# Performance work log

Hardware: AMD Instinct MI355X
Metric: run time of the kernel (lower is better)

Reference implementation:

```python
import jax, jax.numpy as jnp
import numpy as np

_OFF = [(dz, dy, dx) for dz in (-1, 0, 1) for dy in (-1, 0, 1) for dx in (-1, 0, 1)]
_K3 = [(kz, ky, kx) for kz in range(3) for ky in range(3) for kx in range(3)]


def _key(c, dims):
    D, H, W = dims
    return ((c[:, 0].astype(np.int64) * D + c[:, 1]) * H + c[:, 2]) * W + c[:, 3]


def _dedupe(c, dims):
    k = _key(c, dims)
    _, idx = np.unique(k, return_index=True)
    return c[np.sort(idx)]


def _make_lookup(coords, dims):
    D, H, W = dims
    keys = _key(coords, dims)
    order = np.argsort(keys)
    skeys = keys[order]

    def query(qc):
        valid = ((qc[:, 1] >= 0) & (qc[:, 1] < D) & (qc[:, 2] >= 0) & (qc[:, 2] < H)
                 & (qc[:, 3] >= 0) & (qc[:, 3] < W))
        qk = _key(np.where(valid[:, None], qc, 0), dims)
        pos = np.clip(np.searchsorted(skeys, qk), 0, len(skeys) - 1)
        hit = valid & (skeys[pos] == qk)
        return np.where(hit, order[pos], -1).astype(np.int32)
    return query


def _subm_nbr(coords, query):
    nbr = np.empty((len(coords), 27), np.int32)
    for ki, (dz, dy, dx) in enumerate(_OFF):
        qc = coords.copy()
        qc[:, 1] += dz; qc[:, 2] += dy; qc[:, 3] += dx
        nbr[:, ki] = query(qc)
    return nbr


def _down(in_coords, pads, out_dims, in_query):
    # spconv SparseConv3d k=3 s=2: output active set + gather rulebook (in = 2*out - p + k)
    p = np.array(pads)
    cand = []
    for k in _K3:
        t = in_coords[:, 1:] + p - np.array(k)
        m = (t % 2 == 0).all(1)
        o = t[m] // 2
        ok = (o >= 0).all(1) & (o < np.array(out_dims)).all(1)
        cand.append(np.concatenate([in_coords[m][ok][:, :1], o[ok]], 1))
    out_coords = _dedupe(np.concatenate(cand), out_dims)
    nbrd = np.empty((len(out_coords), 27), np.int32)
    for ki, k in enumerate(_K3):
        qc = out_coords.copy()
        qc[:, 1:] = out_coords[:, 1:] * 2 - p + np.array(k)
        nbrd[:, ki] = in_query(qc)
    return out_coords, nbrd


def _inv(in_coords, pads, out_query):
    # inverse conv: for each stride-s input voxel i, gather downsampled voxel o = (i+p-k)/2
    p = np.array(pads)
    nbr = np.full((len(in_coords), 27), -1, np.int32)
    for ki, k in enumerate(_K3):
        t = in_coords[:, 1:] + p - np.array(k)
        div = (t % 2 == 0).all(1)
        qc = in_coords.copy()
        qc[:, 1:] = np.where(div[:, None], t // 2, -1)
        nbr[:, ki] = np.where(div, out_query(qc), -1)
    return nbr


def setup_inputs() -> dict:
    rng = np.random.default_rng(0)
    B, K, P, STD = 4, 160, 128, 3.0
    D1 = (41, 1024, 1024)  # sparse_shape (z, y, x)
    pts = []
    for b in range(B):
        ctr = np.stack([rng.uniform(2, d - 3, K) for d in D1], 1)
        pb = ctr[:, None, :] + rng.normal(0.0, STD, (K, P, 3))
        pb = np.clip(np.rint(pb.reshape(-1, 3)), 0, np.array(D1) - 1).astype(np.int64)
        pts.append(np.concatenate([np.full((len(pb), 1), b, np.int64), pb], 1))
    c1 = _dedupe(np.concatenate(pts), D1)
    D2 = tuple((d + 2 * q - 3) // 2 + 1 for d, q in zip(D1, (1, 1, 1)))
    D3 = tuple((d + 2 * q - 3) // 2 + 1 for d, q in zip(D2, (1, 1, 1)))
    D4 = tuple((d + 2 * q - 3) // 2 + 1 for d, q in zip(D3, (0, 1, 1)))
    q1 = _make_lookup(c1, D1); nbr1 = _subm_nbr(c1, q1)
    c2, nbrd2 = _down(c1, (1, 1, 1), D2, q1); q2 = _make_lookup(c2, D2); nbr2 = _subm_nbr(c2, q2)
    c3, nbrd3 = _down(c2, (1, 1, 1), D3, q2); q3 = _make_lookup(c3, D3); nbr3 = _subm_nbr(c3, q3)
    c4, nbrd4 = _down(c3, (0, 1, 1), D4, q3); q4 = _make_lookup(c4, D4); nbr4 = _subm_nbr(c4, q4)
    nbri4 = _inv(c3, (0, 1, 1), q4)
    nbri3 = _inv(c2, (1, 1, 1), q3)
    nbri2 = _inv(c1, (1, 1, 1), q2)
    N1 = len(c1)
    w = lambda *s: jnp.asarray((0.05 * rng.standard_normal(s)).astype(np.float32))
    bn = lambda n, c: jnp.asarray(np.stack([1.0 + 0.02 * rng.standard_normal((n, c)),
                                            0.02 * rng.standard_normal((n, c))], 1).astype(np.float32))
    return {
        'voxel_feat': jnp.asarray(rng.standard_normal((N1, 4)).astype(np.float32)),
        'Win': w(27, 4, 32),
        'W32': w(10, 27, 32, 32),
        'W64': w(10, 27, 64, 64),
        'Wd3': w(27, 32, 64),
        'W6432': w(3, 27, 64, 32),
        'W12864': w(2, 27, 128, 64),
        'bn32': bn(14, 32),
        'bn64': bn(13, 64),
        'nbr1': jnp.asarray(nbr1), 'nbr2': jnp.asarray(nbr2),
        'nbr3': jnp.asarray(nbr3), 'nbr4': jnp.asarray(nbr4),
        'nbrd2': jnp.asarray(nbrd2), 'nbrd3': jnp.asarray(nbrd3), 'nbrd4': jnp.asarray(nbrd4),
        'nbri4': jnp.asarray(nbri4), 'nbri3': jnp.asarray(nbri3), 'nbri2': jnp.asarray(nbri2),
    }


def _conv(feat, nbr, W):
    # rulebook gather-matmul-scatter: out[n] = sum_k feat[nbr[n,k]] @ W[k]
    out = jnp.zeros((nbr.shape[0], W.shape[-1]), feat.dtype)
    for k in range(27):
        idx = nbr[:, k]
        g = jnp.where((idx >= 0)[:, None], feat[jnp.maximum(idx, 0)], 0.0)
        out = out + g @ W[k]
    return out


def _block(f, nbr, W, sb):  # conv + (folded, eval-mode) BN + ReLU
    return jax.nn.relu(_conv(f, nbr, W) * sb[0] + sb[1])


def _basic(f, nbr, Wa, sa, Wb, sb):  # SparseBasicBlock
    h = jax.nn.relu(_conv(f, nbr, Wa) * sa[0] + sa[1])
    h = _conv(h, nbr, Wb) * sb[0] + sb[1]
    return jax.nn.relu(h + f)


def _reduce(c, oc):  # channel_reduction: view(n, oc, -1).sum(2)
    return c.reshape(c.shape[0], oc, -1).sum(-1)


def _forward(voxel_feat, Win, W32, W64, Wd3, W6432, W12864, bn32, bn64,
             nbr1, nbr2, nbr3, nbr4, nbrd2, nbrd3, nbrd4, nbri4, nbri3, nbri2):
    x = _block(voxel_feat, nbr1, Win, bn32[0])       # conv_input
    x1 = _block(x, nbr1, W32[0], bn32[1])            # conv1
    h = _block(x1, nbrd2, W32[1], bn32[2])           # spconv2 stride-2
    h = _block(h, nbr2, W32[2], bn32[3])
    x2 = _block(h, nbr2, W32[3], bn32[4])
    h = _block(x2, nbrd3, Wd3, bn64[0])              # spconv3 stride-2, 32->64
    h = _block(h, nbr3, W64[0], bn64[1])
    x3 = _block(h, nbr3, W64[1], bn64[2])
    h = _block(x3, nbrd4, W64[2], bn64[3])           # spconv4 stride-2, pad (0,1,1)
    h = _block(h, nbr4, W64[3], bn64[4])
    x4 = _block(h, nbr4, W64[4], bn64[5])
    # UR block 4 (lateral = bottom = x4)
    t = _basic(x4, nbr4, W64[5], bn64[6], W64[6], bn64[7])
    cat = jnp.concatenate([x4, t], 1)                # [N4, 128]
    x = _block(cat, nbr4, W12864[0], bn64[11]) + _reduce(cat, 64)
    xu4 = _block(x, nbri4, W64[7], bn64[8])          # inverseconv -> level 3
    # UR block 3
    t = _basic(x3, nbr3, W64[8], bn64[9], W64[9], bn64[10])
    cat = jnp.concatenate([xu4, t], 1)
    x = _block(cat, nbr3, W12864[1], bn64[12]) + _reduce(cat, 64)
    xu3 = _block(x, nbri3, W6432[0], bn32[11])       # inverseconv -> level 2, 32ch
    # UR block 2
    t = _basic(x2, nbr2, W32[4], bn32[5], W32[5], bn32[6])
    cat = jnp.concatenate([xu3, t], 1)
    x = _block(cat, nbr2, W6432[1], bn32[12]) + _reduce(cat, 32)
    xu2 = _block(x, nbri2, W32[6], bn32[7])          # inverseconv -> level 1
    # UR block 1 (conv_inv = conv5, submanifold at level 1)
    t = _basic(x1, nbr1, W32[7], bn32[8], W32[8], bn32[9])
    cat = jnp.concatenate([xu2, t], 1)
    x = _block(cat, nbr1, W6432[2], bn32[13]) + _reduce(cat, 32)
    return _block(x, nbr1, W32[9], bn32[10])         # conv5 -> unet_voxel_feat [N1, 32]


def reference(voxel_feat, Win, W32, W64, Wd3, W6432, W12864, bn32, bn64,
              nbr1, nbr2, nbr3, nbr4, nbrd2, nbrd3, nbrd4, nbri4, nbri3, nbri2):
    return _forward(voxel_feat, Win, W32, W64, Wd3, W6432, W12864, bn32, bn64,
                    nbr1, nbr2, nbr3, nbr4, nbrd2, nbrd3, nbrd4, nbri4, nbri3, nbri2)
```

## Files before the change

kernel.cpp:

```cpp
#include <hip/hip_runtime.h>


template<int CIN_A, int CIN_B, int COUT, int EPI, bool SPLIT>
__global__ __launch_bounds__(256) void spconv(
    const float* __restrict__ inA,
    const float* __restrict__ inB,
    const int*   __restrict__ nbr,
    const float* __restrict__ W,
    const float* __restrict__ bn,
    const float* __restrict__ skip,
    float*       __restrict__ out,
    float*       __restrict__ pout,
    int N, int KS)
{
    constexpr int CIN   = CIN_A + CIN_B;
    constexpr int BM    = (COUT == 32) ? 128 : 64;
    constexpr int COL_T = COUT / 4;
    constexpr int ROW_T = 256 / COL_T;
    static_assert(ROW_T * 4 == BM, "tile mismatch");
    constexpr int V     = CIN / 4;
    constexpr int GTOT  = BM * V;
    constexpr int GPT   = (GTOT + 255) / 256;
    constexpr int CSTR  = 256 / BM;
    constexpr int WTOT  = CIN * COUT / 4;
    constexpr int WPT   = (WTOT + 255) / 256;

    __shared__ int   s_nbr[BM * 27];
    __shared__ float s_G[CIN][BM];
    __shared__ float s_W[CIN * COUT];

    const int tid = threadIdx.x;
    const int tx  = tid % COL_T;
    const int ty  = tid / COL_T;

    unsigned nwg = gridDim.x;
    unsigned q8 = nwg / 8u, r8 = nwg % 8u;
    unsigned xcd = blockIdx.x % 8u, sub = blockIdx.x / 8u;
    unsigned id = (xcd < r8 ? xcd * (q8 + 1u) : r8 * (q8 + 1u) + (xcd - r8) * q8) + sub;

    int rb, k0, k1, kg;
    if (SPLIT) {
        kg = (int)(id % (unsigned)KS);
        rb = (int)(id / (unsigned)KS);
        int kper = 27 / KS;
        k0 = kg * kper; k1 = k0 + kper;
    } else {
        kg = 0; rb = (int)id; k0 = 0; k1 = 27;
    }
    const int row0 = rb * BM;

    for (int e = tid; e < BM * 27; e += 256) {
        int rr = row0 + e / 27;
        s_nbr[e] = (rr < N) ? nbr[(size_t)row0 * 27 + e] : -1;
    }
    __syncthreads();

    const int gr  = tid % BM;
    const int gc0 = tid / BM;
    float4 gv[GPT];
    float4 wv[WPT];

    auto load_tap = [&](int k) {
        int idx = s_nbr[gr * 27 + k];
        #pragma unroll
        for (int j = 0; j < GPT; ++j) {
            int e = tid + j * 256;
            if ((GTOT % 256 == 0) || e < GTOT) {
                int c4 = gc0 + j * CSTR;
                float4 v = make_float4(0.f, 0.f, 0.f, 0.f);
                if (idx >= 0) {
                    if (CIN_B == 0 || c4 * 4 < CIN_A)
                        v = *(const float4*)(inA + (size_t)idx * CIN_A + c4 * 4);
                    else
                        v = *(const float4*)(inB + (size_t)idx * CIN_B + c4 * 4 - CIN_A);
                }
                gv[j] = v;
            }
        }
        const float4* Wg = (const float4*)(W + (size_t)k * CIN * COUT);
        #pragma unroll
        for (int j = 0; j < WPT; ++j) {
            int e = tid + j * 256;
            if ((WTOT % 256 == 0) || e < WTOT) wv[j] = Wg[e];
        }
    };

    auto store_tap = [&]() {
        #pragma unroll
        for (int j = 0; j < GPT; ++j) {
            int e = tid + j * 256;
            if ((GTOT % 256 == 0) || e < GTOT) {
                int c4 = gc0 + j * CSTR;
                s_G[c4 * 4 + 0][gr] = gv[j].x;
                s_G[c4 * 4 + 1][gr] = gv[j].y;
                s_G[c4 * 4 + 2][gr] = gv[j].z;
                s_G[c4 * 4 + 3][gr] = gv[j].w;
            }
        }
        #pragma unroll
        for (int j = 0; j < WPT; ++j) {
            int e = tid + j * 256;
            if ((WTOT % 256 == 0) || e < WTOT) ((float4*)s_W)[e] = wv[j];
        }
    };

    float acc[4][4] = {};
    load_tap(k0);

    for (int k = k0; k < k1; ++k) {
        __syncthreads();
        store_tap();
        __syncthreads();
        if (k + 1 < k1) load_tap(k + 1);
        #pragma unroll 16
        for (int ci = 0; ci < CIN; ++ci) {
            float4 g = *(const float4*)&s_G[ci][ty * 4];
            float4 w = *(const float4*)&s_W[ci * COUT + tx * 4];
            acc[0][0] += g.x * w.x; acc[0][1] += g.x * w.y; acc[0][2] += g.x * w.z; acc[0][3] += g.x * w.w;
            acc[1][0] += g.y * w.x; acc[1][1] += g.y * w.y; acc[1][2] += g.y * w.z; acc[1][3] += g.y * w.w;
            acc[2][0] += g.z * w.x; acc[2][1] += g.z * w.y; acc[2][2] += g.z * w.z; acc[2][3] += g.z * w.w;
            acc[3][0] += g.w * w.x; acc[3][1] += g.w * w.y; acc[3][2] += g.w * w.z; acc[3][3] += g.w * w.w;
        }
    }

    const int co0 = tx * 4;
    if (SPLIT) {
        #pragma unroll
        for (int i = 0; i < 4; ++i) {
            int rr = row0 + ty * 4 + i;
            if (rr < N) {
                float4 y = make_float4(acc[i][0], acc[i][1], acc[i][2], acc[i][3]);
                *(float4*)(pout + ((size_t)kg * N + rr) * COUT + co0) = y;
            }
        }
    } else {
        float4 sc = *(const float4*)(bn + co0);
        float4 bi = *(const float4*)(bn + COUT + co0);
        #pragma unroll
        for (int i = 0; i < 4; ++i) {
            int rr = row0 + ty * 4 + i;
            if (rr >= N) break;
            float4 y;
            y.x = acc[i][0] * sc.x + bi.x;
            y.y = acc[i][1] * sc.y + bi.y;
            y.z = acc[i][2] * sc.z + bi.z;
            y.w = acc[i][3] * sc.w + bi.w;
            if (EPI == 1) {
                float4 s = *(const float4*)(skip + (size_t)rr * COUT + co0);
                y.x += s.x; y.y += s.y; y.z += s.z; y.w += s.w;
            }
            y.x = fmaxf(y.x, 0.f); y.y = fmaxf(y.y, 0.f);
            y.z = fmaxf(y.z, 0.f); y.w = fmaxf(y.w, 0.f);
            if (EPI == 2) {
                const float* rs = (2 * co0 < CIN_A)
                    ? inA + (size_t)rr * CIN_A + 2 * co0
                    : inB + (size_t)rr * CIN_B + 2 * co0 - CIN_A;
                float4 p0 = ((const float4*)rs)[0];
                float4 p1 = ((const float4*)rs)[1];
                y.x += p0.x + p0.y; y.y += p0.z + p0.w;
                y.z += p1.x + p1.y; y.w += p1.z + p1.w;
            }
            *(float4*)(out + (size_t)rr * COUT + co0) = y;
        }
    }
}

template<int CIN_A, int CIN_B, int COUT, int EPI>
__global__ __launch_bounds__(256) void epi_k(
    const float* __restrict__ P, int KS,
    const float* __restrict__ bn,
    const float* __restrict__ skip,
    const float* __restrict__ inA,
    const float* __restrict__ inB,
    float* __restrict__ out, int N)
{
    int t = blockIdx.x * 256 + threadIdx.x;
    int total = N * (COUT / 4);
    if (t >= total) return;
    int r   = t / (COUT / 4);
    int co0 = (t % (COUT / 4)) * 4;

    float4 y = make_float4(0.f, 0.f, 0.f, 0.f);
    for (int kg = 0; kg < KS; ++kg) {
        float4 p = *(const float4*)(P + ((size_t)kg * N + r) * COUT + co0);
        y.x += p.x; y.y += p.y; y.z += p.z; y.w += p.w;
    }
    float4 sc = *(const float4*)(bn + co0);
    float4 bi = *(const float4*)(bn + COUT + co0);
    y.x = y.x * sc.x + bi.x; y.y = y.y * sc.y + bi.y;
    y.z = y.z * sc.z + bi.z; y.w = y.w * sc.w + bi.w;
    if (EPI == 1) {
        float4 s = *(const float4*)(skip + (size_t)r * COUT + co0);
        y.x += s.x; y.y += s.y; y.z += s.z; y.w += s.w;
    }
    y.x = fmaxf(y.x, 0.f); y.y = fmaxf(y.y, 0.f);
    y.z = fmaxf(y.z, 0.f); y.w = fmaxf(y.w, 0.f);
    if (EPI == 2) {
        const float* rs = (2 * co0 < CIN_A)
            ? inA + (size_t)r * CIN_A + 2 * co0
            : inB + (size_t)r * CIN_B + 2 * co0 - CIN_A;
        float4 p0 = ((const float4*)rs)[0];
        float4 p1 = ((const float4*)rs)[1];
        y.x += p0.x + p0.y; y.y += p0.z + p0.w;
        y.z += p1.x + p1.y; y.w += p1.z + p1.w;
    }
    *(float4*)(out + (size_t)r * COUT + co0) = y;
}

static inline int ksel(int nblk) {
    return nblk >= 512 ? 1 : (nblk >= 170 ? 3 : 9);
}

extern "C" void kernel_launch(void* const* d_in, const int* in_sizes, int n_in,
                              void* d_out, int out_size, void* d_ws, size_t ws_size,
                              hipStream_t stream)
{
    (void)n_in; (void)out_size; (void)ws_size;
    const float* vf     = (const float*)d_in[0];
    const float* Win    = (const float*)d_in[1];
    const float* W32    = (const float*)d_in[2];
    const float* W64    = (const float*)d_in[3];
    const float* Wd3    = (const float*)d_in[4];
    const float* W6432  = (const float*)d_in[5];
    const float* W12864 = (const float*)d_in[6];
    const float* bn32   = (const float*)d_in[7];
    const float* bn64   = (const float*)d_in[8];
    const int* nbr1  = (const int*)d_in[9];
    const int* nbr2  = (const int*)d_in[10];
    const int* nbr3  = (const int*)d_in[11];
    const int* nbr4  = (const int*)d_in[12];
    const int* nbrd2 = (const int*)d_in[13];
    const int* nbrd3 = (const int*)d_in[14];
    const int* nbrd4 = (const int*)d_in[15];
    const int* nbri4 = (const int*)d_in[16];
    const int* nbri3 = (const int*)d_in[17];
    const int* nbri2 = (const int*)d_in[18];

    const int N1 = in_sizes[9]  / 27;
    const int N2 = in_sizes[10] / 27;
    const int N3 = in_sizes[11] / 27;
    const int N4 = in_sizes[12] / 27;

    float* ws = (float*)d_ws;
    size_t off = 0;
    auto alloc = [&](size_t n) { float* p = ws + off; off += n; return p; };
    float* X1  = alloc((size_t)N1 * 32);
    float* TA  = alloc((size_t)N1 * 32);
    float* TA2 = alloc((size_t)N1 * 32);
    float* TU1 = alloc((size_t)N1 * 32);
    float* X2  = alloc((size_t)N2 * 32);
    float* TB2 = alloc((size_t)N2 * 32);
    float* TC2 = alloc((size_t)N2 * 32);
    float* TU2 = alloc((size_t)N2 * 32);
    float* X3  = alloc((size_t)N3 * 64);
    float* TB3 = alloc((size_t)N3 * 64);
    float* TC3 = alloc((size_t)N3 * 64);
    float* TU3 = alloc((size_t)N3 * 64);
    float* X4  = alloc((size_t)N4 * 64);
    float* TB4 = alloc((size_t)N4 * 64);
    float* TC4 = alloc((size_t)N4 * 64);
    float* OUT = (float*)d_out;

    auto pneed = [&](int N, int BM, int CO) -> size_t {
        int nb = (N + BM - 1) / BM; int ks = ksel(nb);
        return ks > 1 ? (size_t)ks * N * CO : 0;
    };
    size_t maxP = 0;
    size_t c;
    c = pneed(N1, 128, 32); if (c > maxP) maxP = c;
    c = pneed(N2, 128, 32); if (c > maxP) maxP = c;
    c = pneed(N3,  64, 64); if (c > maxP) maxP = c;
    c = pneed(N4,  64, 64); if (c > maxP) maxP = c;
    float* P = alloc(maxP);

    const size_t S32 = 27*32*32, S64 = (size_t)27*64*64, S6432 = (size_t)27*64*32, S12864 = (size_t)27*128*64;

#define CONV(CA, CB, CO, EP, pA, pB, pN, pW, pBN, pS, pO, NN) do {                      \
        constexpr int BM_ = ((CO) == 32) ? 128 : 64;                                    \
        int nblk_ = ((NN) + BM_ - 1) / BM_;                                             \
        int ks_ = ksel(nblk_);                                                          \
        if (ks_ == 1) {                                                                 \
            spconv<CA, CB, CO, EP, false><<<dim3((unsigned)nblk_), 256, 0, stream>>>(   \
                pA, pB, pN, pW, pBN, pS, pO, nullptr, NN, 1);                           \
        } else {                                                                        \
            spconv<CA, CB, CO, EP, true><<<dim3((unsigned)(nblk_ * ks_)), 256, 0, stream>>>( \
                pA, pB, pN, pW, pBN, pS, nullptr, P, NN, ks_);                          \
            int tot4_ = (NN) * ((CO) / 4);                                              \
            epi_k<CA, CB, CO, EP><<<dim3((unsigned)((tot4_ + 255) / 256)), 256, 0, stream>>>( \
                P, ks_, pBN, pS, pA, pB, pO, NN);                                       \
        }                                                                               \
    } while (0)

    CONV(4,0,32,0,  vf,  nullptr, nbr1,  Win,         bn32+0*64,  nullptr, TA,  N1);
    CONV(32,0,32,0, TA,  nullptr, nbr1,  W32+0*S32,   bn32+1*64,  nullptr, X1,  N1);
    CONV(32,0,32,0, X1,  nullptr, nbrd2, W32+1*S32,   bn32+2*64,  nullptr, TB2, N2);
    CONV(32,0,32,0, TB2, nullptr, nbr2,  W32+2*S32,   bn32+3*64,  nullptr, TC2, N2);
    CONV(32,0,32,0, TC2, nullptr, nbr2,  W32+3*S32,   bn32+4*64,  nullptr, X2,  N2);
    CONV(32,0,64,0, X2,  nullptr, nbrd3, Wd3,         bn64+0*128, nullptr, TB3, N3);
    CONV(64,0,64,0, TB3, nullptr, nbr3,  W64+0*S64,   bn64+1*128, nullptr, TC3, N3);
    CONV(64,0,64,0, TC3, nullptr, nbr3,  W64+1*S64,   bn64+2*128, nullptr, X3,  N3);
    CONV(64,0,64,0, X3,  nullptr, nbrd4, W64+2*S64,   bn64+3*128, nullptr, TB4, N4);
    CONV(64,0,64,0, TB4, nullptr, nbr4,  W64+3*S64,   bn64+4*128, nullptr, TC4, N4);
    CONV(64,0,64,0, TC4, nullptr, nbr4,  W64+4*S64,   bn64+5*128, nullptr, X4,  N4);
    CONV(64,0,64,0, X4,  nullptr, nbr4,  W64+5*S64,   bn64+6*128, nullptr, TB4, N4);
    CONV(64,0,64,1, TB4, nullptr, nbr4,  W64+6*S64,   bn64+7*128, X4,      TC4, N4);
    CONV(64,64,64,2, X4, TC4,     nbr4,  W12864+0*S12864, bn64+11*128, nullptr, TB4, N4);
    CONV(64,0,64,0, TB4, nullptr, nbri4, W64+7*S64,   bn64+8*128, nullptr, TU3, N3);
    CONV(64,0,64,0, X3,  nullptr, nbr3,  W64+8*S64,   bn64+9*128, nullptr, TB3, N3);
    CONV(64,0,64,1, TB3, nullptr, nbr3,  W64+9*S64,   bn64+10*128, X3,     TC3, N3);
    CONV(64,64,64,2, TU3, TC3,    nbr3,  W12864+1*S12864, bn64+12*128, nullptr, TB3, N3);
    CONV(64,0,32,0, TB3, nullptr, nbri3, W6432+0*S6432, bn32+11*64, nullptr, TU2, N2);
    CONV(32,0,32,0, X2,  nullptr, nbr2,  W32+4*S32,   bn32+5*64,  nullptr, TB2, N2);
    CONV(32,0,32,1, TB2, nullptr, nbr2,  W32+5*S32,   bn32+6*64,  X2,      TC2, N2);
    CONV(32,32,32,2, TU2, TC2,    nbr2,  W6432+1*S6432, bn32+12*64, nullptr, TB2, N2);
    CONV(32,0,32,0, TB2, nullptr, nbri2, W32+6*S32,   bn32+7*64,  nullptr, TU1, N1);
    CONV(32,0,32,0, X1,  nullptr, nbr1,  W32+7*S32,   bn32+8*64,  nullptr, TA,  N1);
    CONV(32,0,32,1, TA,  nullptr, nbr1,  W32+8*S32,   bn32+9*64,  X1,      TA2, N1);
    CONV(32,32,32,2, TU1, TA2,    nbr1,  W6432+2*S6432, bn32+13*64, nullptr, TA,  N1);
    CONV(32,0,32,0, TA,  nullptr, nbr1,  W32+9*S32,   bn32+10*64, nullptr, OUT, N1);
#undef CONV
}
```

Measured before the change: 4.098 ms.

## Switch sparse conv to one-row-per-thread with direct global weight reads

Measured after the change: 4.630 ms. 1.13x slower.

```diff
diff --git a/kernel.cpp b/kernel.cpp
--- a/kernel.cpp
+++ b/kernel.cpp
@@ -13,155 +13,104 @@
     float*       __restrict__ pout,
     int N, int KS)
 {
-    constexpr int CIN   = CIN_A + CIN_B;
-    constexpr int BM    = (COUT == 32) ? 128 : 64;
-    constexpr int COL_T = COUT / 4;
-    constexpr int ROW_T = 256 / COL_T;
-    static_assert(ROW_T * 4 == BM, "tile mismatch");
-    constexpr int V     = CIN / 4;
-    constexpr int GTOT  = BM * V;
-    constexpr int GPT   = (GTOT + 255) / 256;
-    constexpr int CSTR  = 256 / BM;
-    constexpr int WTOT  = CIN * COUT / 4;
-    constexpr int WPT   = (WTOT + 255) / 256;
-
-    __shared__ int   s_nbr[BM * 27];
-    __shared__ float s_G[CIN][BM];
-    __shared__ float s_W[CIN * COUT];
-
-    const int tid = threadIdx.x;
-    const int tx  = tid % COL_T;
-    const int ty  = tid / COL_T;
+    constexpr int CIN = CIN_A + CIN_B;
+    constexpr int NQ  = COUT / 4;
+
+    const int lane = threadIdx.x & 63;
+    const int wid  = threadIdx.x >> 6;
 
     unsigned nwg = gridDim.x;
     unsigned q8 = nwg / 8u, r8 = nwg % 8u;
     unsigned xcd = blockIdx.x % 8u, sub = blockIdx.x / 8u;
     unsigned id = (xcd < r8 ? xcd * (q8 + 1u) : r8 * (q8 + 1u) + (xcd - r8) * q8) + sub;
 
-    int rb, k0, k1, kg;
+    int kg, rb;
+    if (SPLIT) { kg = (int)(id % (unsigned)KS); rb = (int)(id / (unsigned)KS); }
+    else       { kg = 0;  rb = (int)id; }
+    const int kper = SPLIT ? 27 / KS : 27;
+    const int k0 = kg * kper, k1 = k0 + kper;
+
+    const int row = rb * 256 + wid * 64 + lane;
+    const bool rv = row < N;
+    const int* nbrp = nbr + (size_t)row * 27;
+
+    float4 acc[NQ];
+    #pragma unroll
+    for (int q = 0; q < NQ; ++q) acc[q] = make_float4(0.f, 0.f, 0.f, 0.f);
+
+    int idx = rv ? nbrp[k0] : -1;
+    for (int k = k0; k < k1; ++k) {
+        const int nidx = (rv && k + 1 < k1) ? nbrp[k + 1] : -1;
+        const float* wb = W + (size_t)k * CIN * COUT;
+        const float  mk = (idx >= 0) ? 1.f : 0.f;
+        const int    si = (idx >= 0) ? idx : 0;
+
+        auto do4 = [&](float4 g, const float* wci) {
+            g.x *= mk; g.y *= mk; g.z *= mk; g.w *= mk;
+            #pragma unroll
+            for (int j = 0; j < 4; ++j) {
+                const float gv = (&g.x)[j];
+                const float4* wr = (const float4*)(wci + j * COUT);
+                #pragma unroll
+                for (int q = 0; q < NQ; ++q) {
+                    float4 w = wr[q];
+                    acc[q].x += gv * w.x; acc[q].y += gv * w.y;
+                    acc[q].z += gv * w.z; acc[q].w += gv * w.w;
+                }
+            }
+        };
+
+        const float* rA = inA + (size_t)si * CIN_A;
+        #pragma unroll 2
+        for (int c4 = 0; c4 < CIN_A / 4; ++c4)
+            do4(*(const float4*)(rA + c4 * 4), wb + (size_t)(c4 * 4) * COUT);
+        if (CIN_B > 0) {
+            const float* rB = inB + (size_t)si * CIN_B;
+            #pragma unroll 2
+            for (int c4 = 0; c4 < CIN_B / 4; ++c4)
+                do4(*(const float4*)(rB + c4 * 4), wb + (size_t)(CIN_A + c4 * 4) * COUT);
+        }
+        idx = nidx;
+    }
+
     if (SPLIT) {
-        kg = (int)(id % (unsigned)KS);
-        rb = (int)(id / (unsigned)KS);
-        int kper = 27 / KS;
-        k0 = kg * kper; k1 = k0 + kper;
-    } else {
-        kg = 0; rb = (int)id; k0 = 0; k1 = 27;
-    }
-    const int row0 = rb * BM;
-
-    for (int e = tid; e < BM * 27; e += 256) {
-        int rr = row0 + e / 27;
-        s_nbr[e] = (rr < N) ? nbr[(size_t)row0 * 27 + e] : -1;
-    }
-    __syncthreads();
-
-    const int gr  = tid % BM;
-    const int gc0 = tid / BM;
-    float4 gv[GPT];
-    float4 wv[WPT];
-
-    auto load_tap = [&](int k) {
-        int idx = s_nbr[gr * 27 + k];
-        #pragma unroll
-        for (int j = 0; j < GPT; ++j) {
-            int e = tid + j * 256;
-            if ((GTOT % 256 == 0) || e < GTOT) {
-                int c4 = gc0 + j * CSTR;
-                float4 v = make_float4(0.f, 0.f, 0.f, 0.f);
-                if (idx >= 0) {
-                    if (CIN_B == 0 || c4 * 4 < CIN_A)
-                        v = *(const float4*)(inA + (size_t)idx * CIN_A + c4 * 4);
-                    else
-                        v = *(const float4*)(inB + (size_t)idx * CIN_B + c4 * 4 - CIN_A);
-                }
-                gv[j] = v;
-            }
-        }
-        const float4* Wg = (const float4*)(W + (size_t)k * CIN * COUT);
-        #pragma unroll
-        for (int j = 0; j < WPT; ++j) {
-            int e = tid + j * 256;
-            if ((WTOT % 256 == 0) || e < WTOT) wv[j] = Wg[e];
-        }
-    };
-
-    auto store_tap = [&]() {
-        #pragma unroll
-        for (int j = 0; j < GPT; ++j) {
-            int e = tid + j * 256;
-            if ((GTOT % 256 == 0) || e < GTOT) {
-                int c4 = gc0 + j * CSTR;
-                s_G[c4 * 4 + 0][gr] = gv[j].x;
-                s_G[c4 * 4 + 1][gr] = gv[j].y;
-                s_G[c4 * 4 + 2][gr] = gv[j].z;
-                s_G[c4 * 4 + 3][gr] = gv[j].w;
-            }
-        }
-        #pragma unroll
-        for (int j = 0; j < WPT; ++j) {
-            int e = tid + j * 256;
-            if ((WTOT % 256 == 0) || e < WTOT) ((float4*)s_W)[e] = wv[j];
-        }
-    };
-
-    float acc[4][4] = {};
-    load_tap(k0);
-
-    for (int k = k0; k < k1; ++k) {
-        __syncthreads();
-        store_tap();
-        __syncthreads();
-        if (k + 1 < k1) load_tap(k + 1);
-        #pragma unroll 16
-        for (int ci = 0; ci < CIN; ++ci) {
-            float4 g = *(const float4*)&s_G[ci][ty * 4];
-            float4 w = *(const float4*)&s_W[ci * COUT + tx * 4];
-            acc[0][0] += g.x * w.x; acc[0][1] += g.x * w.y; acc[0][2] += g.x * w.z; acc[0][3] += g.x * w.w;
-            acc[1][0] += g.y * w.x; acc[1][1] += g.y * w.y; acc[1][2] += g.y * w.z; acc[1][3] += g.y * w.w;
-            acc[2][0] += g.z * w.x; acc[2][1] += g.z * w.y; acc[2][2] += g.z * w.z; acc[2][3] += g.z * w.w;
-            acc[3][0] += g.w * w.x; acc[3][1] += g.w * w.y; acc[3][2] += g.w * w.z; acc[3][3] += g.w * w.w;
-        }
-    }
-
-    const int co0 = tx * 4;
-    if (SPLIT) {
-        #pragma unroll
-        for (int i = 0; i < 4; ++i) {
-            int rr = row0 + ty * 4 + i;
-            if (rr < N) {
-                float4 y = make_float4(acc[i][0], acc[i][1], acc[i][2], acc[i][3]);
-                *(float4*)(pout + ((size_t)kg * N + rr) * COUT + co0) = y;
-            }
-        }
-    } else {
-        float4 sc = *(const float4*)(bn + co0);
-        float4 bi = *(const float4*)(bn + COUT + co0);
-        #pragma unroll
-        for (int i = 0; i < 4; ++i) {
-            int rr = row0 + ty * 4 + i;
-            if (rr >= N) break;
-            float4 y;
-            y.x = acc[i][0] * sc.x + bi.x;
-            y.y = acc[i][1] * sc.y + bi.y;
-            y.z = acc[i][2] * sc.z + bi.z;
-            y.w = acc[i][3] * sc.w + bi.w;
-            if (EPI == 1) {
-                float4 s = *(const float4*)(skip + (size_t)rr * COUT + co0);
-                y.x += s.x; y.y += s.y; y.z += s.z; y.w += s.w;
-            }
-            y.x = fmaxf(y.x, 0.f); y.y = fmaxf(y.y, 0.f);
-            y.z = fmaxf(y.z, 0.f); y.w = fmaxf(y.w, 0.f);
-            if (EPI == 2) {
-                const float* rs = (2 * co0 < CIN_A)
-                    ? inA + (size_t)rr * CIN_A + 2 * co0
-                    : inB + (size_t)rr * CIN_B + 2 * co0 - CIN_A;
-                float4 p0 = ((const float4*)rs)[0];
-                float4 p1 = ((const float4*)rs)[1];
-                y.x += p0.x + p0.y; y.y += p0.z + p0.w;
-                y.z += p1.x + p1.y; y.w += p1.z + p1.w;
-            }
-            *(float4*)(out + (size_t)rr * COUT + co0) = y;
-        }
+        if (rv) {
+            float* pp = pout + ((size_t)kg * N + row) * COUT;
+            #pragma unroll
+            for (int q = 0; q < NQ; ++q) *(float4*)(pp + q * 4) = acc[q];
+        }
+        return;
+    }
+    if (!rv) return;
+
+    float*       op   = out + (size_t)row * COUT;
+    const float* skp  = (EPI == 1) ? skip + (size_t)row * COUT : nullptr;
+    const float* catA = inA + (size_t)row * CIN_A;
+    const float* catB = (CIN_B > 0) ? inB + (size_t)row * CIN_B : nullptr;
+
+    #pragma unroll
+    for (int q = 0; q < NQ; ++q) {
+        float4 sc = *(const float4*)(bn + q * 4);
+        float4 bi = *(const float4*)(bn + COUT + q * 4);
+        float4 y;
+        y.x = acc[q].x * sc.x + bi.x;
+        y.y = acc[q].y * sc.y + bi.y;
+        y.z = acc[q].z * sc.z + bi.z;
+        y.w = acc[q].w * sc.w + bi.w;
+        if (EPI == 1) {
+            float4 s = *(const float4*)(skp + q * 4);
+            y.x += s.x; y.y += s.y; y.z += s.z; y.w += s.w;
+        }
+        y.x = fmaxf(y.x, 0.f); y.y = fmaxf(y.y, 0.f);
+        y.z = fmaxf(y.z, 0.f); y.w = fmaxf(y.w, 0.f);
+        if (EPI == 2) {
+            const float* rs = (8 * q < CIN_A) ? catA + 8 * q : catB + 8 * q - CIN_A;
+            float4 p0 = ((const float4*)rs)[0];
+            float4 p1 = ((const float4*)rs)[1];
+            y.x += p0.x + p0.y; y.y += p0.z + p0.w;
+            y.z += p1.x + p1.y; y.w += p1.z + p1.w;
+        }
+        *(float4*)(op + q * 4) = y;
     }
 }
 
@@ -207,15 +156,20 @@
     *(float4*)(out + (size_t)r * COUT + co0) = y;
 }
 
-static inline int ksel(int nblk) {
-    return nblk >= 512 ? 1 : (nblk >= 170 ? 3 : 9);
+static inline int ksel(int nblk, int N, int CO, size_t prem_elems) {
+    int ks = 27;
+    if (nblk >= 600) ks = 1;
+    else if (nblk * 3 >= 600) ks = 3;
+    else if (nblk * 9 >= 600) ks = 9;
+    while (ks > 1 && (size_t)ks * (size_t)N * (size_t)CO > prem_elems) ks /= 3;
+    return ks;
 }
 
 extern "C" void kernel_launch(void* const* d_in, const int* in_sizes, int n_in,
                               void* d_out, int out_size, void* d_ws, size_t ws_size,
                               hipStream_t stream)
 {
-    (void)n_in; (void)out_size; (void)ws_size;
+    (void)n_in; (void)out_size;
     const float* vf     = (const float*)d_in[0];
     const float* Win    = (const float*)d_in[1];
     const float* W32    = (const float*)d_in[2];
@@ -261,24 +215,14 @@
     float* TC4 = alloc((size_t)N4 * 64);
     float* OUT = (float*)d_out;
 
-    auto pneed = [&](int N, int BM, int CO) -> size_t {
-        int nb = (N + BM - 1) / BM; int ks = ksel(nb);
-        return ks > 1 ? (size_t)ks * N * CO : 0;
-    };
-    size_t maxP = 0;
-    size_t c;
-    c = pneed(N1, 128, 32); if (c > maxP) maxP = c;
-    c = pneed(N2, 128, 32); if (c > maxP) maxP = c;
-    c = pneed(N3,  64, 64); if (c > maxP) maxP = c;
-    c = pneed(N4,  64, 64); if (c > maxP) maxP = c;
-    float* P = alloc(maxP);
+    size_t prem = (ws_size / 4 > off + 1024) ? (ws_size / 4 - off - 1024) : 0;
+    float* P = ws + off;
 
     const size_t S32 = 27*32*32, S64 = (size_t)27*64*64, S6432 = (size_t)27*64*32, S12864 = (size_t)27*128*64;
 
 #define CONV(CA, CB, CO, EP, pA, pB, pN, pW, pBN, pS, pO, NN) do {                      \
-        constexpr int BM_ = ((CO) == 32) ? 128 : 64;                                    \
-        int nblk_ = ((NN) + BM_ - 1) / BM_;                                             \
-        int ks_ = ksel(nblk_);                                                          \
+        int nblk_ = ((NN) + 255) / 256;                                                 \
+        int ks_ = ksel(nblk_, (NN), (CO), prem);                                        \
         if (ks_ == 1) {                                                                 \
             spconv<CA, CB, CO, EP, false><<<dim3((unsigned)nblk_), 256, 0, stream>>>(   \
                 pA, pB, pN, pW, pBN, pS, pO, nullptr, NN, 1);                           \
```
